# Optimization experiments

Measured on AMD Instinct MI355X. Metric: run time of the kernel, lower is better.

The kernel has to match this reference:

```python
import jax, jax.numpy as jnp
import numpy as np

N = 100000
E = 3200000
IN_DIM = 128
HD = 64
HEADS = 4
NEG_SLOPE = 0.2


def setup_inputs() -> dict:
    key = jax.random.key(0)
    ks = jax.random.split(key, 12)
    s = lambda fan_in: 1.0 / np.sqrt(fan_in)
    x = jax.random.normal(ks[0], (N, IN_DIM), dtype=jnp.float32)
    edge_index = jax.random.randint(ks[1], (2, E), 0, N, dtype=jnp.int64)
    W1 = jax.random.normal(ks[2], (IN_DIM, HEADS * HD), dtype=jnp.float32) * s(IN_DIM)
    a_src1 = jax.random.normal(ks[3], (HEADS, HD), dtype=jnp.float32) * s(HD)
    a_dst1 = jax.random.normal(ks[4], (HEADS, HD), dtype=jnp.float32) * s(HD)
    b1 = jnp.zeros((HEADS * HD,), dtype=jnp.float32)
    W2 = jax.random.normal(ks[5], (HEADS * HD, HD), dtype=jnp.float32) * s(HEADS * HD)
    a_src2 = jax.random.normal(ks[6], (1, HD), dtype=jnp.float32) * s(HD)
    a_dst2 = jax.random.normal(ks[7], (1, HD), dtype=jnp.float32) * s(HD)
    b2 = jnp.zeros((HD,), dtype=jnp.float32)
    lin_w = jax.random.normal(ks[8], (HD, 2), dtype=jnp.float32) * s(HD)
    lin_b = jnp.zeros((2,), dtype=jnp.float32)
    return {"x": x, "edge_index": edge_index, "W1": W1, "a_src1": a_src1,
            "a_dst1": a_dst1, "b1": b1, "W2": W2, "a_src2": a_src2,
            "a_dst2": a_dst2, "b2": b2, "lin_w": lin_w, "lin_b": lin_b}


def gat_conv(x, src, dst, W, a_src, a_dst, bias, heads, out_dim, concat):
    n = x.shape[0]
    h = (x @ W).reshape(n, heads, out_dim)                 # [N,H,D]
    alpha_s = jnp.einsum('nhd,hd->nh', h, a_src)           # [N,H]
    alpha_d = jnp.einsum('nhd,hd->nh', h, a_dst)           # [N,H]
    e = alpha_s[src] + alpha_d[dst]                        # [Etot,H]
    e = jnp.where(e > 0, e, NEG_SLOPE * e)                 # leaky relu
    m = jax.ops.segment_max(e, dst, num_segments=n)        # scatter-softmax (stable)
    m = jnp.where(jnp.isfinite(m), m, 0.0)
    e = jnp.exp(e - m[dst])
    denom = jax.ops.segment_sum(e, dst, num_segments=n)
    alpha = e / denom[dst]                                 # [Etot,H]
    out = jax.ops.segment_sum(h[src] * alpha[:, :, None], dst, num_segments=n)  # [N,H,D]
    out = out.reshape(n, heads * out_dim) if concat else out.mean(axis=1)
    return out + bias


def reference(x, edge_index, W1, a_src1, a_dst1, b1, W2, a_src2, a_dst2, b2, lin_w, lin_b):
    n = x.shape[0]
    loops = jnp.arange(n, dtype=edge_index.dtype)
    src = jnp.concatenate([edge_index[0], loops])          # add self-loops (PyG default)
    dst = jnp.concatenate([edge_index[1], loops])
    h = gat_conv(x, src, dst, W1, a_src1, a_dst1, b1, HEADS, HD, True)
    h = jax.nn.elu(h)
    h = gat_conv(h, src, dst, W2, a_src2, a_dst2, b2, 1, HD, True)
    h = jax.nn.elu(h)
    return h @ lin_w + lin_b                               # [N,2]
```

## Files before the change

kernel.cpp:

```cpp
#include <hip/hip_runtime.h>
#include <hip/hip_fp16.h>
#include <math.h>

#define NN 100000
#define EE 3200000
#define ETOT (EE + NN)
#define NEG_SLOPE 0.2f
#define DMAX 96
#define CHUNK 4096
#define NB0 ((ETOT + CHUNK - 1) / CHUNK)
#define RB 391
#define CAP 16384
#define PREPB 391

typedef _Float16 half8 __attribute__((ext_vector_type(8)));
typedef _Float16 half4v __attribute__((ext_vector_type(4)));
typedef _Float16 half2v __attribute__((ext_vector_type(2)));
typedef float floatx4 __attribute__((ext_vector_type(4)));

__device__ __forceinline__ float wsum64(float v) {
#pragma unroll
  for (int o = 32; o; o >>= 1) v += __shfl_xor(v, o);
  return v;
}
__device__ __forceinline__ float lrelu(float v) { return v > 0.f ? v : NEG_SLOPE * v; }
__device__ __forceinline__ float elu1(float v) { return v > 0.f ? v : expm1f(v); }

__global__ void k_init(int* __restrict__ ccur) {
  ccur[threadIdx.x] = threadIdx.x * CAP;
}

__global__ __launch_bounds__(256) void k_pass1(const int* __restrict__ ei,
                                               int* __restrict__ ccur,
                                               unsigned* __restrict__ ebuf,
                                               const float* __restrict__ W1,
                                               const float* __restrict__ W2,
                                               _Float16* __restrict__ W1t,
                                               _Float16* __restrict__ W2t,
                                               const float* __restrict__ x,
                                               const float* __restrict__ a_src1,
                                               const float* __restrict__ a_dst1,
                                               _Float16* __restrict__ xh,
                                               float* __restrict__ as1,
                                               float* __restrict__ ad1) {
  __shared__ __align__(16) char smem[26624];
  const int b = blockIdx.x;
  const int t = threadIdx.x;
  if (b < NB0) {
    unsigned* vv = (unsigned*)smem;
    unsigned short* cbv = (unsigned short*)(smem + 16384);
    int* h = (int*)(smem + 24576);
    int* cur = (int*)(smem + 25600);
    h[t] = 0;
    __syncthreads();
    int base = b * CHUNK;
    int lim = base + CHUNK; if (lim > ETOT) lim = ETOT;
    int cnt = lim - base;
    for (int i = t; i < cnt; i += 256) {
      int e = base + i;
      int s, d;
      if (e < EE) { s = ei[e]; d = ei[EE + e]; } else { s = e - EE; d = s; }
      unsigned cb = (unsigned)d / (unsigned)RB;
      unsigned dloc = (unsigned)d - cb * (unsigned)RB;
      vv[i] = (dloc << 17) | (unsigned)s;
      cbv[i] = (unsigned short)cb;
      atomicAdd(&h[cb], 1);
    }
    __syncthreads();
    if (h[t]) cur[t] = atomicAdd(&ccur[t], h[t]);
    __syncthreads();
    for (int i = t; i < cnt; i += 256) {
      int cb = cbv[i];
      int pos = atomicAdd(&cur[cb], 1);
      ebuf[pos] = vv[i];
    }
    return;
  }
  if (b < NB0 + 192) {
    int idx = (b - NB0) * 256 + t;
    if (idx < 32768) {
      int n = idx >> 7, k = idx & 127;
      W1t[idx] = (_Float16)W1[k * 256 + n];
    } else {
      int j = idx - 32768;
      int n = j >> 8, k = j & 255;
      W2t[j] = (_Float16)W2[k * 64 + n];
    }
    return;
  }
  float* vs = (float*)smem;
  float* vd = vs + 512;
  for (int i = t; i < 512; i += 256) {
    int h = i >> 7, k = i & 127;
    const float* wrow = W1 + (size_t)k * 256 + h * 64;
    float ss = 0.f, dd = 0.f;
#pragma unroll 8
    for (int d2 = 0; d2 < 64; ++d2) {
      float wv = wrow[d2];
      ss = fmaf(wv, a_src1[h * 64 + d2], ss);
      dd = fmaf(wv, a_dst1[h * 64 + d2], dd);
    }
    vs[i] = ss; vd[i] = dd;
  }
  __syncthreads();
  const int lane = t & 63;
  const int gw = (b - NB0 - 192) * 4 + (t >> 6);
  for (int n = gw; n < NN; n += 4 * PREPB) {
    float2 xv = *(const float2*)(x + (size_t)n * 128 + lane * 2);
    half2v hx; hx[0] = (_Float16)xv.x; hx[1] = (_Float16)xv.y;
    *(half2v*)(xh + (size_t)n * 128 + lane * 2) = hx;
    float p[8];
#pragma unroll
    for (int h = 0; h < 4; ++h) {
      p[h]     = xv.x * vs[h * 128 + lane * 2] + xv.y * vs[h * 128 + lane * 2 + 1];
      p[4 + h] = xv.x * vd[h * 128 + lane * 2] + xv.y * vd[h * 128 + lane * 2 + 1];
    }
#pragma unroll
    for (int j = 0; j < 8; ++j) p[j] = wsum64(p[j]);
    if (lane == 0) {
      *(float4*)(as1 + n * 4) = make_float4(p[0], p[1], p[2], p[3]);
      *(float4*)(ad1 + n * 4) = make_float4(p[4], p[5], p[6], p[7]);
    }
  }
}

__global__ __launch_bounds__(256) void k_pass2(const unsigned* __restrict__ ebuf,
                                               const int* __restrict__ ccur,
                                               int* __restrict__ offs,
                                               int* __restrict__ degarr,
                                               int* __restrict__ csr) {
  __shared__ unsigned ed[CAP];
  __shared__ int hist[RB];
  __shared__ int cur[RB];
  int b = blockIdx.x, t = threadIdx.x;
  int d0 = b * RB;
  int rb = NN - d0; if (rb > RB) rb = RB;
  int w0 = b * CAP;
  int cnt = ccur[b] - w0;
  if (cnt > CAP) cnt = CAP;
  for (int j = t; j < rb; j += 256) hist[j] = 0;
  __syncthreads();
  for (int i = t; i < cnt; i += 256) {
    unsigned v = ebuf[w0 + i];
    ed[i] = v;
    atomicAdd(&hist[v >> 17], 1);
  }
  __syncthreads();
  if (t == 0) {
    int run = w0;
    for (int j = 0; j < rb; ++j) { cur[j] = run; run += hist[j]; }
  }
  __syncthreads();
  for (int j = t; j < rb; j += 256) {
    offs[d0 + j] = cur[j];
    degarr[d0 + j] = hist[j];
  }
  __syncthreads();
  for (int i = t; i < cnt; i += 256) {
    unsigned v = ed[i];
    int pos = atomicAdd(&cur[v >> 17], 1);
    csr[pos] = (int)(v & 0x1FFFFu);
  }
}

__global__ __launch_bounds__(256) void k_agg1(const int* __restrict__ offs,
                                              const int* __restrict__ degarr,
                                              const int* __restrict__ csr_src,
                                              const float* __restrict__ a_s,
                                              const float* __restrict__ a_d,
                                              const _Float16* __restrict__ xh,
                                              _Float16* __restrict__ agg) {
  __shared__ __align__(16) float alp[4][DMAX][4];
  __shared__ int sidx[4][DMAX];
  const int wid = threadIdx.x >> 6;
  const int n = blockIdx.x * 4 + wid;
  const int lane = threadIdx.x & 63;
  const int beg = offs[n], deg = degarr[n];
  const float4 ad = *(const float4*)(a_d + n * 4);
  float4 sm = make_float4(0.f, 0.f, 0.f, 0.f);
  for (int d = lane; d < deg; d += 64) {
    int s = csr_src[beg + d];
    float4 as = *(const float4*)(a_s + s * 4);
    float e0 = __expf(lrelu(as.x + ad.x));
    float e1 = __expf(lrelu(as.y + ad.y));
    float e2 = __expf(lrelu(as.z + ad.z));
    float e3 = __expf(lrelu(as.w + ad.w));
    sm.x += e0; sm.y += e1; sm.z += e2; sm.w += e3;
    if (d < DMAX) {
      sidx[wid][d] = s;
      *(float4*)&alp[wid][d][0] = make_float4(e0, e1, e2, e3);
    }
  }
  sm.x = wsum64(sm.x); sm.y = wsum64(sm.y); sm.z = wsum64(sm.z); sm.w = wsum64(sm.w);
  const float4 inv4 = make_float4(1.f / sm.x, 1.f / sm.y, 1.f / sm.z, 1.f / sm.w);
  const int dlim = deg < DMAX ? deg : DMAX;
  for (int d = lane; d < dlim; d += 64) {
    float4 a = *(float4*)&alp[wid][d][0];
    a.x *= inv4.x; a.y *= inv4.y; a.z *= inv4.z; a.w *= inv4.w;
    *(float4*)&alp[wid][d][0] = a;
  }
  const int g = lane >> 4;
  const int sub = lane & 15;
  const _Float16* __restrict__ hb = xh + sub * 8;
  float acc[4][8];
#pragma unroll
  for (int h = 0; h < 4; ++h)
#pragma unroll
    for (int j = 0; j < 8; ++j) acc[h][j] = 0.f;
  int d = 0;
  for (; d + 8 <= dlim; d += 8) {
    int i0 = d + g, i1 = d + 4 + g;
    int s0 = sidx[wid][i0], s1 = sidx[wid][i1];
    float4 w0 = *(float4*)&alp[wid][i0][0];
    float4 w1 = *(float4*)&alp[wid][i1][0];
    half8 r0 = *(const half8*)(hb + (size_t)s0 * 128);
    half8 r1 = *(const half8*)(hb + (size_t)s1 * 128);
#pragma unroll
    for (int j = 0; j < 8; ++j) {
      float f0 = (float)r0[j], f1 = (float)r1[j];
      acc[0][j] = fmaf(f0, w0.x, acc[0][j]);
      acc[1][j] = fmaf(f0, w0.y, acc[1][j]);
      acc[2][j] = fmaf(f0, w0.z, acc[2][j]);
      acc[3][j] = fmaf(f0, w0.w, acc[3][j]);
      acc[0][j] = fmaf(f1, w1.x, acc[0][j]);
      acc[1][j] = fmaf(f1, w1.y, acc[1][j]);
      acc[2][j] = fmaf(f1, w1.z, acc[2][j]);
      acc[3][j] = fmaf(f1, w1.w, acc[3][j]);
    }
  }
  if (d + 4 <= dlim) {
    int i0 = d + g;
    int s0 = sidx[wid][i0];
    float4 w0 = *(float4*)&alp[wid][i0][0];
    half8 r0 = *(const half8*)(hb + (size_t)s0 * 128);
#pragma unroll
    for (int j = 0; j < 8; ++j) {
      float f0 = (float)r0[j];
      acc[0][j] = fmaf(f0, w0.x, acc[0][j]);
      acc[1][j] = fmaf(f0, w0.y, acc[1][j]);
      acc[2][j] = fmaf(f0, w0.z, acc[2][j]);
      acc[3][j] = fmaf(f0, w0.w, acc[3][j]);
    }
    d += 4;
  }
  if (d < dlim) {
    int idx = d + g;
    bool v = idx < dlim;
    int s = sidx[wid][v ? idx : d];
    float4 w0 = *(float4*)&alp[wid][v ? idx : d][0];
    if (!v) { w0.x = 0.f; w0.y = 0.f; w0.z = 0.f; w0.w = 0.f; }
    half8 r0 = *(const half8*)(hb + (size_t)s * 128);
#pragma unroll
    for (int j = 0; j < 8; ++j) {
      float f0 = (float)r0[j];
      acc[0][j] = fmaf(f0, w0.x, acc[0][j]);
      acc[1][j] = fmaf(f0, w0.y, acc[1][j]);
      acc[2][j] = fmaf(f0, w0.z, acc[2][j]);
      acc[3][j] = fmaf(f0, w0.w, acc[3][j]);
    }
  }
  if (deg > DMAX) {
    for (int dd = DMAX + g; dd < deg; dd += 4) {
      int s = csr_src[beg + dd];
      float4 as = *(const float4*)(a_s + s * 4);
      float w0x = __expf(lrelu(as.x + ad.x)) * inv4.x;
      float w0y = __expf(lrelu(as.y + ad.y)) * inv4.y;
      float w0z = __expf(lrelu(as.z + ad.z)) * inv4.z;
      float w0w = __expf(lrelu(as.w + ad.w)) * inv4.w;
      half8 r0 = *(const half8*)(hb + (size_t)s * 128);
#pragma unroll
      for (int j = 0; j < 8; ++j) {
        float f0 = (float)r0[j];
        acc[0][j] = fmaf(f0, w0x, acc[0][j]);
        acc[1][j] = fmaf(f0, w0y, acc[1][j]);
        acc[2][j] = fmaf(f0, w0z, acc[2][j]);
        acc[3][j] = fmaf(f0, w0w, acc[3][j]);
      }
    }
  }
#pragma unroll
  for (int h = 0; h < 4; ++h)
#pragma unroll
    for (int j = 0; j < 8; ++j) {
      acc[h][j] += __shfl_xor(acc[h][j], 16);
      acc[h][j] += __shfl_xor(acc[h][j], 32);
    }
  if (g == 0) {
#pragma unroll
    for (int h = 0; h < 4; ++h) {
      half8 o;
#pragma unroll
      for (int j = 0; j < 8; ++j) o[j] = (_Float16)acc[h][j];
      *(half8*)(agg + ((size_t)n * 4 + h) * 128 + sub * 8) = o;
    }
  }
}

__global__ __launch_bounds__(256) void k_gemmAgg2(const _Float16* __restrict__ agg,
                                                  const _Float16* __restrict__ W1t,
                                                  const _Float16* __restrict__ W2t,
                                                  const float* __restrict__ b1,
                                                  const float* __restrict__ a_src2,
                                                  const float* __restrict__ a_dst2,
                                                  _Float16* __restrict__ h2h,
                                                  float* __restrict__ as_out,
                                                  float* __restrict__ ad_out) {
  __shared__ _Float16 h1eT[64][264];
  const int tid = threadIdx.x;
  const int row0 = blockIdx.x * 64;
  const int wid = tid >> 6, lane = tid & 63;
  const int m16 = lane & 15, quad = lane >> 4;
  floatx4 acc1[4][4];
#pragma unroll
  for (int h = 0; h < 4; ++h)
#pragma unroll
    for (int nt = 0; nt < 4; ++nt) acc1[h][nt] = (floatx4){0.f, 0.f, 0.f, 0.f};
  const size_t arow = (size_t)(row0 + wid * 16 + m16) * 512;
#pragma unroll
  for (int h = 0; h < 4; ++h) {
#pragma unroll
    for (int ks = 0; ks < 4; ++ks) {
      half8 av = *(const half8*)(agg + arow + h * 128 + ks * 32 + quad * 8);
#pragma unroll
      for (int nt = 0; nt < 4; ++nt) {
        half8 bv = *(const half8*)(W1t + (size_t)(h * 64 + nt * 16 + m16) * 128 + ks * 32 + quad * 8);
        acc1[h][nt] = __builtin_amdgcn_mfma_f32_16x16x32_f16(av, bv, acc1[h][nt], 0, 0, 0);
      }
    }
  }
#pragma unroll
  for (int h = 0; h < 4; ++h)
#pragma unroll
    for (int nt = 0; nt < 4; ++nt) {
      float bb = b1[h * 64 + nt * 16 + m16];
#pragma unroll
      for (int r = 0; r < 4; ++r)
        h1eT[wid * 16 + quad * 4 + r][h * 64 + nt * 16 + m16] = (_Float16)elu1(acc1[h][nt][r] + bb);
    }
  __syncthreads();
  floatx4 acc2[4];
#pragma unroll
  for (int nt = 0; nt < 4; ++nt) acc2[nt] = (floatx4){0.f, 0.f, 0.f, 0.f};
#pragma unroll
  for (int ks = 0; ks < 8; ++ks) {
    half8 av = *(const half8*)&h1eT[wid * 16 + m16][ks * 32 + quad * 8];
#pragma unroll
    for (int nt = 0; nt < 4; ++nt) {
      half8 bv = *(const half8*)(W2t + (size_t)(nt * 16 + m16) * 256 + ks * 32 + quad * 8);
      acc2[nt] = __builtin_amdgcn_mfma_f32_16x16x32_f16(av, bv, acc2[nt], 0, 0, 0);
    }
  }
  float asr[4], adr[4];
#pragma unroll
  for (int nt = 0; nt < 4; ++nt) {
    asr[nt] = a_src2[nt * 16 + m16];
    adr[nt] = a_dst2[nt * 16 + m16];
  }
#pragma unroll
  for (int r = 0; r < 4; ++r) {
    float ps = 0.f, pd = 0.f;
#pragma unroll
    for (int nt = 0; nt < 4; ++nt) {
      ps = fmaf(acc2[nt][r], asr[nt], ps);
      pd = fmaf(acc2[nt][r], adr[nt], pd);
    }
#pragma unroll
    for (int o = 1; o < 16; o <<= 1) { ps += __shfl_xor(ps, o); pd += __shfl_xor(pd, o); }
    int gr = row0 + wid * 16 + quad * 4 + r;
    if (gr < NN) {
      if (m16 == 0) { as_out[gr] = ps; ad_out[gr] = pd; }
#pragma unroll
      for (int nt = 0; nt < 4; ++nt)
        h2h[(size_t)gr * 64 + nt * 16 + m16] = (_Float16)acc2[nt][r];
    }
  }
}

__global__ __launch_bounds__(256) void k_attn2(const int* __restrict__ offs,
                                               const int* __restrict__ degarr,
                                               const int* __restrict__ csr_src,
                                               const float* __restrict__ a_s,
                                               const float* __restrict__ a_d,
                                               const _Float16* __restrict__ h2h,
                                               const float* __restrict__ b2,
                                               const float* __restrict__ lin_w,
                                               const float* __restrict__ lin_b,
                                               float* __restrict__ out) {
  __shared__ float alpha2[4][DMAX];
  __shared__ int sidx2[4][DMAX];
  const int wid = threadIdx.x >> 6;
  const int n = blockIdx.x * 4 + wid;
  const int lane = threadIdx.x & 63;
  const int beg = offs[n], deg = degarr[n];
  const float adn = a_d[n];
  float sm = 0.f;
  for (int d = lane; d < deg; d += 64) {
    int s = csr_src[beg + d];
    float e = __expf(lrelu(a_s[s] + adn));
    sm += e;
    if (d < DMAX) { sidx2[wid][d] = s; alpha2[wid][d] = e; }
  }
  sm = wsum64(sm);
  const float inv = 1.f / sm;
  const int dlim = deg < DMAX ? deg : DMAX;
  for (int d = lane; d < dlim; d += 64) alpha2[wid][d] *= inv;
  const int g = lane >> 4;
  const int sub = lane & 15;
  const _Float16* __restrict__ hb = h2h + sub * 4;
  float a0 = 0.f, a1 = 0.f, a2 = 0.f, a3 = 0.f;
  int d = 0;
  for (; d + 8 <= dlim; d += 8) {
    int i0 = d + g, i1 = d + 4 + g;
    int s0 = sidx2[wid][i0], s1 = sidx2[wid][i1];
    float w0 = alpha2[wid][i0], w1 = alpha2[wid][i1];
    half4v r0 = *(const half4v*)(hb + (size_t)s0 * 64);
    half4v r1 = *(const half4v*)(hb + (size_t)s1 * 64);
    a0 = fmaf((float)r0[0], w0, a0); a1 = fmaf((float)r0[1], w0, a1);
    a2 = fmaf((float)r0[2], w0, a2); a3 = fmaf((float)r0[3], w0, a3);
    a0 = fmaf((float)r1[0], w1, a0); a1 = fmaf((float)r1[1], w1, a1);
    a2 = fmaf((float)r1[2], w1, a2); a3 = fmaf((float)r1[3], w1, a3);
  }
  if (d + 4 <= dlim) {
    int i0 = d + g;
    int s0 = sidx2[wid][i0];
    float w0 = alpha2[wid][i0];
    half4v r0 = *(const half4v*)(hb + (size_t)s0 * 64);
    a0 = fmaf((float)r0[0], w0, a0); a1 = fmaf((float)r0[1], w0, a1);
    a2 = fmaf((float)r0[2], w0, a2); a3 = fmaf((float)r0[3], w0, a3);
    d += 4;
  }
  if (d < dlim) {
    int idx = d + g;
    bool v = idx < dlim;
    int s = sidx2[wid][v ? idx : d];
    float w = v ? alpha2[wid][idx] : 0.f;
    half4v r = *(const half4v*)(hb + (size_t)s * 64);
    a0 = fmaf((float)r[0], w, a0); a1 = fmaf((float)r[1], w, a1);
    a2 = fmaf((float)r[2], w, a2); a3 = fmaf((float)r[3], w, a3);
  }
  if (deg > DMAX && g == 0) {
    for (int dd = DMAX; dd < deg; ++dd) {
      int s = csr_src[beg + dd];
      float w = __expf(lrelu(a_s[s] + adn)) * inv;
      half4v r = *(const half4v*)(hb + (size_t)s * 64);
      a0 = fmaf((float)r[0], w, a0); a1 = fmaf((float)r[1], w, a1);
      a2 = fmaf((float)r[2], w, a2); a3 = fmaf((float)r[3], w, a3);
    }
  }
  a0 += __shfl_xor(a0, 16); a1 += __shfl_xor(a1, 16);
  a2 += __shfl_xor(a2, 16); a3 += __shfl_xor(a3, 16);
  a0 += __shfl_xor(a0, 32); a1 += __shfl_xor(a1, 32);
  a2 += __shfl_xor(a2, 32); a3 += __shfl_xor(a3, 32);
  const int c = sub * 4;
  float4 bb = *(const float4*)(b2 + c);
  float o0 = elu1(a0 + bb.x);
  float o1 = elu1(a1 + bb.y);
  float o2 = elu1(a2 + bb.z);
  float o3 = elu1(a3 + bb.w);
  float4 lw0 = *(const float4*)(lin_w + c * 2);
  float4 lw1 = *(const float4*)(lin_w + c * 2 + 4);
  float p0 = o0 * lw0.x + o1 * lw0.z + o2 * lw1.x + o3 * lw1.z;
  float p1 = o0 * lw0.y + o1 * lw0.w + o2 * lw1.y + o3 * lw1.w;
  p0 = wsum64(p0) * 0.25f;
  p1 = wsum64(p1) * 0.25f;
  if (lane == 0) {
    out[n * 2 + 0] = p0 + lin_b[0];
    out[n * 2 + 1] = p1 + lin_b[1];
  }
}

extern "C" void kernel_launch(void* const* d_in, const int* in_sizes, int n_in,
                              void* d_out, int out_size, void* d_ws, size_t ws_size,
                              hipStream_t stream) {
  const float* x      = (const float*)d_in[0];
  const int*   ei     = (const int*)d_in[1];
  const float* W1     = (const float*)d_in[2];
  const float* a_src1 = (const float*)d_in[3];
  const float* a_dst1 = (const float*)d_in[4];
  const float* b1     = (const float*)d_in[5];
  const float* W2     = (const float*)d_in[6];
  const float* a_src2 = (const float*)d_in[7];
  const float* a_dst2 = (const float*)d_in[8];
  const float* b2     = (const float*)d_in[9];
  const float* lin_w  = (const float*)d_in[10];
  const float* lin_b  = (const float*)d_in[11];
  float* outp = (float*)d_out;

  char* w = (char*)d_ws;
  _Float16* agg  = (_Float16*)(w + 0);
  unsigned* ebuf = (unsigned*)(w + 33554432);
  _Float16* xh   = (_Float16*)(w + 102432768);
  _Float16* h2h  = (_Float16*)(w + 102432768);
  int*    csr    = (int*)(w + 128032768);
  _Float16* W1t  = (_Float16*)(w + 144809984);
  _Float16* W2t  = (_Float16*)(w + 144875520);
  float*  as1    = (float*)(w + 144908288);
  float*  ad1    = (float*)(w + 146508288);
  float*  as2    = (float*)(w + 148108288);
  float*  ad2    = (float*)(w + 148508288);
  int*    offs   = (int*)(w + 148908288);
  int*    degarr = (int*)(w + 149308288);
  int*    ccur   = (int*)(w + 149708288);

  k_init<<<1, 256, 0, stream>>>(ccur);
  k_pass1<<<NB0 + 192 + PREPB, 256, 0, stream>>>(ei, ccur, ebuf, W1, W2, W1t, W2t,
                                                 x, a_src1, a_dst1, xh, as1, ad1);
  k_pass2<<<256, 256, 0, stream>>>(ebuf, ccur, offs, degarr, csr);

  k_agg1<<<NN / 4, 256, 0, stream>>>(offs, degarr, csr, as1, ad1, xh, agg);
  k_gemmAgg2<<<1563, 256, 0, stream>>>(agg, W1t, W2t, b1, a_src2, a_dst2, h2h, as2, ad2);

  k_attn2<<<NN / 4, 256, 0, stream>>>(offs, degarr, csr, as2, ad2, h2h, b2, lin_w, lin_b, outp);
}
```

Before: 594.2 us.

## Fuse layer-1 aggregation with both dense GEMMs into one kernel via LDS

```diff
diff --git a/kernel.cpp b/kernel.cpp
--- a/kernel.cpp
+++ b/kernel.cpp
@@ -163,216 +163,198 @@
   }
 }
 
-__global__ __launch_bounds__(256) void k_agg1(const int* __restrict__ offs,
-                                              const int* __restrict__ degarr,
-                                              const int* __restrict__ csr_src,
-                                              const float* __restrict__ a_s,
-                                              const float* __restrict__ a_d,
-                                              const _Float16* __restrict__ xh,
-                                              _Float16* __restrict__ agg) {
+__global__ __launch_bounds__(256) void k_fused1(const int* __restrict__ offs,
+                                                const int* __restrict__ degarr,
+                                                const int* __restrict__ csr_src,
+                                                const float* __restrict__ a_s,
+                                                const float* __restrict__ a_d,
+                                                const _Float16* __restrict__ xh,
+                                                const _Float16* __restrict__ W1t,
+                                                const _Float16* __restrict__ W2t,
+                                                const float* __restrict__ b1,
+                                                const float* __restrict__ a_src2,
+                                                const float* __restrict__ a_dst2,
+                                                _Float16* __restrict__ h2h,
+                                                float* __restrict__ as_out,
+                                                float* __restrict__ ad_out) {
   __shared__ __align__(16) float alp[4][DMAX][4];
   __shared__ int sidx[4][DMAX];
+  __shared__ __align__(16) _Float16 aggT[16][520];
+  __shared__ __align__(16) _Float16 h1eT[16][264];
+  __shared__ float prt[2][4][16];
   const int wid = threadIdx.x >> 6;
-  const int n = blockIdx.x * 4 + wid;
   const int lane = threadIdx.x & 63;
-  const int beg = offs[n], deg = degarr[n];
-  const float4 ad = *(const float4*)(a_d + n * 4);
-  float4 sm = make_float4(0.f, 0.f, 0.f, 0.f);
-  for (int d = lane; d < deg; d += 64) {
-    int s = csr_src[beg + d];
-    float4 as = *(const float4*)(a_s + s * 4);
-    float e0 = __expf(lrelu(as.x + ad.x));
-    float e1 = __expf(lrelu(as.y + ad.y));
-    float e2 = __expf(lrelu(as.z + ad.z));
-    float e3 = __expf(lrelu(as.w + ad.w));
-    sm.x += e0; sm.y += e1; sm.z += e2; sm.w += e3;
-    if (d < DMAX) {
-      sidx[wid][d] = s;
-      *(float4*)&alp[wid][d][0] = make_float4(e0, e1, e2, e3);
-    }
-  }
-  sm.x = wsum64(sm.x); sm.y = wsum64(sm.y); sm.z = wsum64(sm.z); sm.w = wsum64(sm.w);
-  const float4 inv4 = make_float4(1.f / sm.x, 1.f / sm.y, 1.f / sm.z, 1.f / sm.w);
-  const int dlim = deg < DMAX ? deg : DMAX;
-  for (int d = lane; d < dlim; d += 64) {
-    float4 a = *(float4*)&alp[wid][d][0];
-    a.x *= inv4.x; a.y *= inv4.y; a.z *= inv4.z; a.w *= inv4.w;
-    *(float4*)&alp[wid][d][0] = a;
-  }
+  const int n0 = blockIdx.x * 16;
   const int g = lane >> 4;
   const int sub = lane & 15;
   const _Float16* __restrict__ hb = xh + sub * 8;
-  float acc[4][8];
-#pragma unroll
-  for (int h = 0; h < 4; ++h)
-#pragma unroll
-    for (int j = 0; j < 8; ++j) acc[h][j] = 0.f;
-  int d = 0;
-  for (; d + 8 <= dlim; d += 8) {
-    int i0 = d + g, i1 = d + 4 + g;
-    int s0 = sidx[wid][i0], s1 = sidx[wid][i1];
-    float4 w0 = *(float4*)&alp[wid][i0][0];
-    float4 w1 = *(float4*)&alp[wid][i1][0];
-    half8 r0 = *(const half8*)(hb + (size_t)s0 * 128);
-    half8 r1 = *(const half8*)(hb + (size_t)s1 * 128);
-#pragma unroll
-    for (int j = 0; j < 8; ++j) {
-      float f0 = (float)r0[j], f1 = (float)r1[j];
-      acc[0][j] = fmaf(f0, w0.x, acc[0][j]);
-      acc[1][j] = fmaf(f0, w0.y, acc[1][j]);
-      acc[2][j] = fmaf(f0, w0.z, acc[2][j]);
-      acc[3][j] = fmaf(f0, w0.w, acc[3][j]);
-      acc[0][j] = fmaf(f1, w1.x, acc[0][j]);
-      acc[1][j] = fmaf(f1, w1.y, acc[1][j]);
-      acc[2][j] = fmaf(f1, w1.z, acc[2][j]);
-      acc[3][j] = fmaf(f1, w1.w, acc[3][j]);
-    }
-  }
-  if (d + 4 <= dlim) {
-    int i0 = d + g;
-    int s0 = sidx[wid][i0];
-    float4 w0 = *(float4*)&alp[wid][i0][0];
-    half8 r0 = *(const half8*)(hb + (size_t)s0 * 128);
-#pragma unroll
-    for (int j = 0; j < 8; ++j) {
-      float f0 = (float)r0[j];
-      acc[0][j] = fmaf(f0, w0.x, acc[0][j]);
-      acc[1][j] = fmaf(f0, w0.y, acc[1][j]);
-      acc[2][j] = fmaf(f0, w0.z, acc[2][j]);
-      acc[3][j] = fmaf(f0, w0.w, acc[3][j]);
-    }
-    d += 4;
-  }
-  if (d < dlim) {
-    int idx = d + g;
-    bool v = idx < dlim;
-    int s = sidx[wid][v ? idx : d];
-    float4 w0 = *(float4*)&alp[wid][v ? idx : d][0];
-    if (!v) { w0.x = 0.f; w0.y = 0.f; w0.z = 0.f; w0.w = 0.f; }
-    half8 r0 = *(const half8*)(hb + (size_t)s * 128);
-#pragma unroll
-    for (int j = 0; j < 8; ++j) {
-      float f0 = (float)r0[j];
-      acc[0][j] = fmaf(f0, w0.x, acc[0][j]);
-      acc[1][j] = fmaf(f0, w0.y, acc[1][j]);
-      acc[2][j] = fmaf(f0, w0.z, acc[2][j]);
-      acc[3][j] = fmaf(f0, w0.w, acc[3][j]);
-    }
-  }
-  if (deg > DMAX) {
-    for (int dd = DMAX + g; dd < deg; dd += 4) {
-      int s = csr_src[beg + dd];
+
+  for (int dn = 0; dn < 4; ++dn) {
+    const int n = n0 + wid * 4 + dn;
+    const int beg = offs[n], deg = degarr[n];
+    const float4 ad = *(const float4*)(a_d + n * 4);
+    float4 sm = make_float4(0.f, 0.f, 0.f, 0.f);
+    for (int d = lane; d < deg; d += 64) {
+      int s = csr_src[beg + d];
       float4 as = *(const float4*)(a_s + s * 4);
-      float w0x = __expf(lrelu(as.x + ad.x)) * inv4.x;
-      float w0y = __expf(lrelu(as.y + ad.y)) * inv4.y;
-      float w0z = __expf(lrelu(as.z + ad.z)) * inv4.z;
-      float w0w = __expf(lrelu(as.w + ad.w)) * inv4.w;
-      half8 r0 = *(const half8*)(hb + (size_t)s * 128);
+      float e0 = __expf(lrelu(as.x + ad.x));
+      float e1 = __expf(lrelu(as.y + ad.y));
+      float e2 = __expf(lrelu(as.z + ad.z));
+      float e3 = __expf(lrelu(as.w + ad.w));
+      sm.x += e0; sm.y += e1; sm.z += e2; sm.w += e3;
+      if (d < DMAX) {
+        sidx[wid][d] = s;
+        *(float4*)&alp[wid][d][0] = make_float4(e0, e1, e2, e3);
+      }
+    }
+    sm.x = wsum64(sm.x); sm.y = wsum64(sm.y); sm.z = wsum64(sm.z); sm.w = wsum64(sm.w);
+    const float4 inv4 = make_float4(1.f / sm.x, 1.f / sm.y, 1.f / sm.z, 1.f / sm.w);
+    const int dlim = deg < DMAX ? deg : DMAX;
+    for (int d = lane; d < dlim; d += 64) {
+      float4 a = *(float4*)&alp[wid][d][0];
+      a.x *= inv4.x; a.y *= inv4.y; a.z *= inv4.z; a.w *= inv4.w;
+      *(float4*)&alp[wid][d][0] = a;
+    }
+    float acc[4][8];
+#pragma unroll
+    for (int h = 0; h < 4; ++h)
+#pragma unroll
+      for (int j = 0; j < 8; ++j) acc[h][j] = 0.f;
+    int d = 0;
+    for (; d + 8 <= dlim; d += 8) {
+      int i0 = d + g, i1 = d + 4 + g;
+      int s0 = sidx[wid][i0], s1 = sidx[wid][i1];
+      float4 w0 = *(float4*)&alp[wid][i0][0];
+      float4 w1 = *(float4*)&alp[wid][i1][0];
+      half8 r0 = *(const half8*)(hb + (size_t)s0 * 128);
+      half8 r1 = *(const half8*)(hb + (size_t)s1 * 128);
+#pragma unroll
+      for (int j = 0; j < 8; ++j) {
+        float f0 = (float)r0[j], f1 = (float)r1[j];
+        acc[0][j] = fmaf(f0, w0.x, acc[0][j]);
+        acc[1][j] = fmaf(f0, w0.y, acc[1][j]);
+        acc[2][j] = fmaf(f0, w0.z, acc[2][j]);
+        acc[3][j] = fmaf(f0, w0.w, acc[3][j]);
+        acc[0][j] = fmaf(f1, w1.x, acc[0][j]);
+        acc[1][j] = fmaf(f1, w1.y, acc[1][j]);
+        acc[2][j] = fmaf(f1, w1.z, acc[2][j]);
+        acc[3][j] = fmaf(f1, w1.w, acc[3][j]);
+      }
+    }
+    if (d + 4 <= dlim) {
+      int i0 = d + g;
+      int s0 = sidx[wid][i0];
+      float4 w0 = *(float4*)&alp[wid][i0][0];
+      half8 r0 = *(const half8*)(hb + (size_t)s0 * 128);
 #pragma unroll
       for (int j = 0; j < 8; ++j) {
         float f0 = (float)r0[j];
-        acc[0][j] = fmaf(f0, w0x, acc[0][j]);
-        acc[1][j] = fmaf(f0, w0y, acc[1][j]);
-        acc[2][j] = fmaf(f0, w0z, acc[2][j]);
-        acc[3][j] = fmaf(f0, w0w, acc[3][j]);
-      }
-    }
-  }
-#pragma unroll
-  for (int h = 0; h < 4; ++h)
-#pragma unroll
-    for (int j = 0; j < 8; ++j) {
-      acc[h][j] += __shfl_xor(acc[h][j], 16);
-      acc[h][j] += __shfl_xor(acc[h][j], 32);
-    }
-  if (g == 0) {
-#pragma unroll
-    for (int h = 0; h < 4; ++h) {
-      half8 o;
-#pragma unroll
-      for (int j = 0; j < 8; ++j) o[j] = (_Float16)acc[h][j];
-      *(half8*)(agg + ((size_t)n * 4 + h) * 128 + sub * 8) = o;
-    }
-  }
-}
-
-__global__ __launch_bounds__(256) void k_gemmAgg2(const _Float16* __restrict__ agg,
-                                                  const _Float16* __restrict__ W1t,
-                                                  const _Float16* __restrict__ W2t,
-                                                  const float* __restrict__ b1,
-                                                  const float* __restrict__ a_src2,
-                                                  const float* __restrict__ a_dst2,
-                                                  _Float16* __restrict__ h2h,
-                                                  float* __restrict__ as_out,
-                                                  float* __restrict__ ad_out) {
-  __shared__ _Float16 h1eT[64][264];
-  const int tid = threadIdx.x;
-  const int row0 = blockIdx.x * 64;
-  const int wid = tid >> 6, lane = tid & 63;
-  const int m16 = lane & 15, quad = lane >> 4;
-  floatx4 acc1[4][4];
-#pragma unroll
-  for (int h = 0; h < 4; ++h)
-#pragma unroll
-    for (int nt = 0; nt < 4; ++nt) acc1[h][nt] = (floatx4){0.f, 0.f, 0.f, 0.f};
-  const size_t arow = (size_t)(row0 + wid * 16 + m16) * 512;
-#pragma unroll
-  for (int h = 0; h < 4; ++h) {
-#pragma unroll
-    for (int ks = 0; ks < 4; ++ks) {
-      half8 av = *(const half8*)(agg + arow + h * 128 + ks * 32 + quad * 8);
-#pragma unroll
-      for (int nt = 0; nt < 4; ++nt) {
-        half8 bv = *(const half8*)(W1t + (size_t)(h * 64 + nt * 16 + m16) * 128 + ks * 32 + quad * 8);
-        acc1[h][nt] = __builtin_amdgcn_mfma_f32_16x16x32_f16(av, bv, acc1[h][nt], 0, 0, 0);
-      }
-    }
-  }
-#pragma unroll
-  for (int h = 0; h < 4; ++h)
+        acc[0][j] = fmaf(f0, w0.x, acc[0][j]);
+        acc[1][j] = fmaf(f0, w0.y, acc[1][j]);
+        acc[2][j] = fmaf(f0, w0.z, acc[2][j]);
+        acc[3][j] = fmaf(f0, w0.w, acc[3][j]);
+      }
+      d += 4;
+    }
+    if (d < dlim) {
+      int idx = d + g;
+      bool v = idx < dlim;
+      int s = sidx[wid][v ? idx : d];
+      float4 w0 = *(float4*)&alp[wid][v ? idx : d][0];
+      if (!v) { w0.x = 0.f; w0.y = 0.f; w0.z = 0.f; w0.w = 0.f; }
+      half8 r0 = *(const half8*)(hb + (size_t)s * 128);
+#pragma unroll
+      for (int j = 0; j < 8; ++j) {
+        float f0 = (float)r0[j];
+        acc[0][j] = fmaf(f0, w0.x, acc[0][j]);
+        acc[1][j] = fmaf(f0, w0.y, acc[1][j]);
+        acc[2][j] = fmaf(f0, w0.z, acc[2][j]);
+        acc[3][j] = fmaf(f0, w0.w, acc[3][j]);
+      }
+    }
+    if (deg > DMAX) {
+      for (int dd = DMAX + g; dd < deg; dd += 4) {
+        int s = csr_src[beg + dd];
+        float4 as = *(const float4*)(a_s + s * 4);
+        float w0x = __expf(lrelu(as.x + ad.x)) * inv4.x;
+        float w0y = __expf(lrelu(as.y + ad.y)) * inv4.y;
+        float w0z = __expf(lrelu(as.z + ad.z)) * inv4.z;
+        float w0w = __expf(lrelu(as.w + ad.w)) * inv4.w;
+        half8 r0 = *(const half8*)(hb + (size_t)s * 128);
+#pragma unroll
+        for (int j = 0; j < 8; ++j) {
+          float f0 = (float)r0[j];
+          acc[0][j] = fmaf(f0, w0x, acc[0][j]);
+          acc[1][j] = fmaf(f0, w0y, acc[1][j]);
+          acc[2][j] = fmaf(f0, w0z, acc[2][j]);
+          acc[3][j] = fmaf(f0, w0w, acc[3][j]);
+        }
+      }
+    }
+#pragma unroll
+    for (int h = 0; h < 4; ++h)
+#pragma unroll
+      for (int j = 0; j < 8; ++j) {
+        acc[h][j] += __shfl_xor(acc[h][j], 16);
+        acc[h][j] += __shfl_xor(acc[h][j], 32);
+      }
+    if (g == 0) {
+#pragma unroll
+      for (int h = 0; h < 4; ++h) {
+        half8 o;
+#pragma unroll
+        for (int j = 0; j < 8; ++j) o[j] = (_Float16)acc[h][j];
+        *(half8*)&aggT[wid * 4 + dn][h * 128 + sub * 8] = o;
+      }
+    }
+  }
+  __syncthreads();
+
+  const int m16 = sub, quad = g;
+  floatx4 acc1[4];
+#pragma unroll
+  for (int nt = 0; nt < 4; ++nt) acc1[nt] = (floatx4){0.f, 0.f, 0.f, 0.f};
+#pragma unroll
+  for (int ks = 0; ks < 4; ++ks) {
+    half8 av = *(half8*)&aggT[m16][wid * 128 + ks * 32 + quad * 8];
 #pragma unroll
     for (int nt = 0; nt < 4; ++nt) {
-      float bb = b1[h * 64 + nt * 16 + m16];
-#pragma unroll
-      for (int r = 0; r < 4; ++r)
-        h1eT[wid * 16 + quad * 4 + r][h * 64 + nt * 16 + m16] = (_Float16)elu1(acc1[h][nt][r] + bb);
-    }
-  __syncthreads();
-  floatx4 acc2[4];
-#pragma unroll
-  for (int nt = 0; nt < 4; ++nt) acc2[nt] = (floatx4){0.f, 0.f, 0.f, 0.f};
+      half8 bv = *(const half8*)(W1t + (size_t)(wid * 64 + nt * 16 + m16) * 128 + ks * 32 + quad * 8);
+      acc1[nt] = __builtin_amdgcn_mfma_f32_16x16x32_f16(av, bv, acc1[nt], 0, 0, 0);
+    }
+  }
+#pragma unroll
+  for (int nt = 0; nt < 4; ++nt) {
+    float bb = b1[wid * 64 + nt * 16 + m16];
+#pragma unroll
+    for (int r = 0; r < 4; ++r)
+      h1eT[quad * 4 + r][wid * 64 + nt * 16 + m16] = (_Float16)elu1(acc1[nt][r] + bb);
+  }
+  __syncthreads();
+
+  floatx4 acc2 = (floatx4){0.f, 0.f, 0.f, 0.f};
 #pragma unroll
   for (int ks = 0; ks < 8; ++ks) {
-    half8 av = *(const half8*)&h1eT[wid * 16 + m16][ks * 32 + quad * 8];
-#pragma unroll
-    for (int nt = 0; nt < 4; ++nt) {
-      half8 bv = *(const half8*)(W2t + (size_t)(nt * 16 + m16) * 256 + ks * 32 + quad * 8);
-      acc2[nt] = __builtin_amdgcn_mfma_f32_16x16x32_f16(av, bv, acc2[nt], 0, 0, 0);
-    }
-  }
-  float asr[4], adr[4];
-#pragma unroll
-  for (int nt = 0; nt < 4; ++nt) {
-    asr[nt] = a_src2[nt * 16 + m16];
-    adr[nt] = a_dst2[nt * 16 + m16];
-  }
+    half8 av = *(half8*)&h1eT[m16][ks * 32 + quad * 8];
+    half8 bv = *(const half8*)(W2t + (size_t)(wid * 16 + m16) * 256 + ks * 32 + quad * 8);
+    acc2 = __builtin_amdgcn_mfma_f32_16x16x32_f16(av, bv, acc2, 0, 0, 0);
+  }
+  const float a2v = a_src2[wid * 16 + m16];
+  const float d2v = a_dst2[wid * 16 + m16];
 #pragma unroll
   for (int r = 0; r < 4; ++r) {
-    float ps = 0.f, pd = 0.f;
-#pragma unroll
-    for (int nt = 0; nt < 4; ++nt) {
-      ps = fmaf(acc2[nt][r], asr[nt], ps);
-      pd = fmaf(acc2[nt][r], adr[nt], pd);
-    }
+    int row = quad * 4 + r;
+    h2h[(size_t)(n0 + row) * 64 + wid * 16 + m16] = (_Float16)acc2[r];
+    float ps = acc2[r] * a2v, pd = acc2[r] * d2v;
 #pragma unroll
     for (int o = 1; o < 16; o <<= 1) { ps += __shfl_xor(ps, o); pd += __shfl_xor(pd, o); }
-    int gr = row0 + wid * 16 + quad * 4 + r;
-    if (gr < NN) {
-      if (m16 == 0) { as_out[gr] = ps; ad_out[gr] = pd; }
-#pragma unroll
-      for (int nt = 0; nt < 4; ++nt)
-        h2h[(size_t)gr * 64 + nt * 16 + m16] = (_Float16)acc2[nt][r];
-    }
+    if (m16 == 0) { prt[0][wid][row] = ps; prt[1][wid][row] = pd; }
+  }
+  __syncthreads();
+  if (threadIdx.x < 16) {
+    int row = threadIdx.x;
+    as_out[n0 + row] = prt[0][0][row] + prt[0][1][row] + prt[0][2][row] + prt[0][3][row];
+    ad_out[n0 + row] = prt[1][0][row] + prt[1][1][row] + prt[1][2][row] + prt[1][3][row];
   }
 }
 
@@ -487,28 +469,27 @@
   float* outp = (float*)d_out;
 
   char* w = (char*)d_ws;
-  _Float16* agg  = (_Float16*)(w + 0);
-  unsigned* ebuf = (unsigned*)(w + 33554432);
-  _Float16* xh   = (_Float16*)(w + 102432768);
-  _Float16* h2h  = (_Float16*)(w + 102432768);
-  int*    csr    = (int*)(w + 128032768);
-  _Float16* W1t  = (_Float16*)(w + 144809984);
-  _Float16* W2t  = (_Float16*)(w + 144875520);
-  float*  as1    = (float*)(w + 144908288);
-  float*  ad1    = (float*)(w + 146508288);
-  float*  as2    = (float*)(w + 148108288);
-  float*  ad2    = (float*)(w + 148508288);
-  int*    offs   = (int*)(w + 148908288);
-  int*    degarr = (int*)(w + 149308288);
-  int*    ccur   = (int*)(w + 149708288);
+  _Float16* xh   = (_Float16*)(w + 0);
+  _Float16* h2h  = (_Float16*)(w + 25600000);
+  unsigned* ebuf = (unsigned*)(w + 38400000);
+  int*    csr    = (int*)(w + 55177216);
+  _Float16* W1t  = (_Float16*)(w + 71954432);
+  _Float16* W2t  = (_Float16*)(w + 72019968);
+  float*  as1    = (float*)(w + 72052736);
+  float*  ad1    = (float*)(w + 73652736);
+  float*  as2    = (float*)(w + 75252736);
+  float*  ad2    = (float*)(w + 75652736);
+  int*    offs   = (int*)(w + 76052736);
+  int*    degarr = (int*)(w + 76452736);
+  int*    ccur   = (int*)(w + 76852736);
 
   k_init<<<1, 256, 0, stream>>>(ccur);
   k_pass1<<<NB0 + 192 + PREPB, 256, 0, stream>>>(ei, ccur, ebuf, W1, W2, W1t, W2t,
                                                  x, a_src1, a_dst1, xh, as1, ad1);
   k_pass2<<<256, 256, 0, stream>>>(ebuf, ccur, offs, degarr, csr);
 
-  k_agg1<<<NN / 4, 256, 0, stream>>>(offs, degarr, csr, as1, ad1, xh, agg);
-  k_gemmAgg2<<<1563, 256, 0, stream>>>(agg, W1t, W2t, b1, a_src2, a_dst2, h2h, as2, ad2);
+  k_fused1<<<NN / 16, 256, 0, stream>>>(offs, degarr, csr, as1, ad1, xh,
+                                        W1t, W2t, b1, a_src2, a_dst2, h2h, as2, ad2);
 
   k_attn2<<<NN / 4, 256, 0, stream>>>(offs, degarr, csr, as2, ad2, h2h, b2, lin_w, lin_b, outp);
 }
```

Result: faster. 551.7 us (-7.2%).

## Restructure gemmAgg2 into 32-row tiles staged in LDS and vectorize x prep

Applied to the files above, without the earlier changes.

```diff
diff --git a/kernel.cpp b/kernel.cpp
--- a/kernel.cpp
+++ b/kernel.cpp
@@ -15,7 +15,6 @@
 
 typedef _Float16 half8 __attribute__((ext_vector_type(8)));
 typedef _Float16 half4v __attribute__((ext_vector_type(4)));
-typedef _Float16 half2v __attribute__((ext_vector_type(2)));
 typedef float floatx4 __attribute__((ext_vector_type(4)));
 
 __device__ __forceinline__ float wsum64(float v) {
@@ -104,20 +103,44 @@
   }
   __syncthreads();
   const int lane = t & 63;
+  const int sub8 = lane >> 3;
+  const int dl = lane & 7;
   const int gw = (b - NB0 - 192) * 4 + (t >> 6);
-  for (int n = gw; n < NN; n += 4 * PREPB) {
-    float2 xv = *(const float2*)(x + (size_t)n * 128 + lane * 2);
-    half2v hx; hx[0] = (_Float16)xv.x; hx[1] = (_Float16)xv.y;
-    *(half2v*)(xh + (size_t)n * 128 + lane * 2) = hx;
+  for (int nb = gw * 8; nb < NN; nb += 4 * PREPB * 8) {
+    const int n = nb + sub8;
+    const bool ok = n < NN;
+    float4 xv[4];
+#pragma unroll
+    for (int j = 0; j < 4; ++j)
+      xv[j] = ok ? *(const float4*)(x + (size_t)n * 128 + dl * 16 + j * 4)
+                 : make_float4(0.f, 0.f, 0.f, 0.f);
+    const float* xf = (const float*)xv;
+    if (ok) {
+      half8 h0, h1;
+#pragma unroll
+      for (int c = 0; c < 8; ++c) { h0[c] = (_Float16)xf[c]; h1[c] = (_Float16)xf[8 + c]; }
+      *(half8*)(xh + (size_t)n * 128 + dl * 16) = h0;
+      *(half8*)(xh + (size_t)n * 128 + dl * 16 + 8) = h1;
+    }
     float p[8];
 #pragma unroll
     for (int h = 0; h < 4; ++h) {
-      p[h]     = xv.x * vs[h * 128 + lane * 2] + xv.y * vs[h * 128 + lane * 2 + 1];
-      p[4 + h] = xv.x * vd[h * 128 + lane * 2] + xv.y * vd[h * 128 + lane * 2 + 1];
-    }
-#pragma unroll
-    for (int j = 0; j < 8; ++j) p[j] = wsum64(p[j]);
-    if (lane == 0) {
+      float ss = 0.f, dd = 0.f;
+#pragma unroll
+      for (int c = 0; c < 16; ++c) {
+        float xc = xf[c];
+        ss = fmaf(xc, vs[h * 128 + dl * 16 + c], ss);
+        dd = fmaf(xc, vd[h * 128 + dl * 16 + c], dd);
+      }
+      p[h] = ss; p[4 + h] = dd;
+    }
+#pragma unroll
+    for (int j = 0; j < 8; ++j) {
+      p[j] += __shfl_xor(p[j], 1);
+      p[j] += __shfl_xor(p[j], 2);
+      p[j] += __shfl_xor(p[j], 4);
+    }
+    if (ok && dl == 0) {
       *(float4*)(as1 + n * 4) = make_float4(p[0], p[1], p[2], p[3]);
       *(float4*)(ad1 + n * 4) = make_float4(p[4], p[5], p[6], p[7]);
     }
@@ -305,74 +328,77 @@
                                                   _Float16* __restrict__ h2h,
                                                   float* __restrict__ as_out,
                                                   float* __restrict__ ad_out) {
-  __shared__ _Float16 h1eT[64][264];
+  __shared__ __align__(16) _Float16 As[32][520];
+  __shared__ __align__(16) _Float16 h1eT[32][264];
+  __shared__ float prt[2][4][32];
   const int tid = threadIdx.x;
-  const int row0 = blockIdx.x * 64;
+  const int row0 = blockIdx.x * 32;
+#pragma unroll
+  for (int i = 0; i < 8; ++i) {
+    int c = i * 256 + tid;
+    int r = c >> 6;
+    int c8 = c & 63;
+    *(half8*)&As[r][c8 * 8] = *(const half8*)(agg + (size_t)(row0 + r) * 512 + c8 * 8);
+  }
+  __syncthreads();
   const int wid = tid >> 6, lane = tid & 63;
   const int m16 = lane & 15, quad = lane >> 4;
-  floatx4 acc1[4][4];
-#pragma unroll
-  for (int h = 0; h < 4; ++h)
-#pragma unroll
-    for (int nt = 0; nt < 4; ++nt) acc1[h][nt] = (floatx4){0.f, 0.f, 0.f, 0.f};
-  const size_t arow = (size_t)(row0 + wid * 16 + m16) * 512;
-#pragma unroll
-  for (int h = 0; h < 4; ++h) {
+  floatx4 acc1[2][4];
+#pragma unroll
+  for (int mt = 0; mt < 2; ++mt)
+#pragma unroll
+    for (int nt = 0; nt < 4; ++nt) acc1[mt][nt] = (floatx4){0.f, 0.f, 0.f, 0.f};
+#pragma unroll
+  for (int mt = 0; mt < 2; ++mt) {
 #pragma unroll
     for (int ks = 0; ks < 4; ++ks) {
-      half8 av = *(const half8*)(agg + arow + h * 128 + ks * 32 + quad * 8);
+      half8 av = *(half8*)&As[mt * 16 + m16][wid * 128 + ks * 32 + quad * 8];
 #pragma unroll
       for (int nt = 0; nt < 4; ++nt) {
-        half8 bv = *(const half8*)(W1t + (size_t)(h * 64 + nt * 16 + m16) * 128 + ks * 32 + quad * 8);
-        acc1[h][nt] = __builtin_amdgcn_mfma_f32_16x16x32_f16(av, bv, acc1[h][nt], 0, 0, 0);
+        half8 bv = *(const half8*)(W1t + (size_t)(wid * 64 + nt * 16 + m16) * 128 + ks * 32 + quad * 8);
+        acc1[mt][nt] = __builtin_amdgcn_mfma_f32_16x16x32_f16(av, bv, acc1[mt][nt], 0, 0, 0);
       }
     }
   }
 #pragma unroll
-  for (int h = 0; h < 4; ++h)
+  for (int mt = 0; mt < 2; ++mt)
 #pragma unroll
     for (int nt = 0; nt < 4; ++nt) {
-      float bb = b1[h * 64 + nt * 16 + m16];
+      float bb = b1[wid * 64 + nt * 16 + m16];
 #pragma unroll
       for (int r = 0; r < 4; ++r)
-        h1eT[wid * 16 + quad * 4 + r][h * 64 + nt * 16 + m16] = (_Float16)elu1(acc1[h][nt][r] + bb);
-    }
-  __syncthreads();
-  floatx4 acc2[4];
-#pragma unroll
-  for (int nt = 0; nt < 4; ++nt) acc2[nt] = (floatx4){0.f, 0.f, 0.f, 0.f};
-#pragma unroll
-  for (int ks = 0; ks < 8; ++ks) {
-    half8 av = *(const half8*)&h1eT[wid * 16 + m16][ks * 32 + quad * 8];
-#pragma unroll
-    for (int nt = 0; nt < 4; ++nt) {
-      half8 bv = *(const half8*)(W2t + (size_t)(nt * 16 + m16) * 256 + ks * 32 + quad * 8);
-      acc2[nt] = __builtin_amdgcn_mfma_f32_16x16x32_f16(av, bv, acc2[nt], 0, 0, 0);
-    }
-  }
-  float asr[4], adr[4];
-#pragma unroll
-  for (int nt = 0; nt < 4; ++nt) {
-    asr[nt] = a_src2[nt * 16 + m16];
-    adr[nt] = a_dst2[nt * 16 + m16];
-  }
-#pragma unroll
-  for (int r = 0; r < 4; ++r) {
-    float ps = 0.f, pd = 0.f;
-#pragma unroll
-    for (int nt = 0; nt < 4; ++nt) {
-      ps = fmaf(acc2[nt][r], asr[nt], ps);
-      pd = fmaf(acc2[nt][r], adr[nt], pd);
-    }
-#pragma unroll
-    for (int o = 1; o < 16; o <<= 1) { ps += __shfl_xor(ps, o); pd += __shfl_xor(pd, o); }
-    int gr = row0 + wid * 16 + quad * 4 + r;
-    if (gr < NN) {
-      if (m16 == 0) { as_out[gr] = ps; ad_out[gr] = pd; }
-#pragma unroll
-      for (int nt = 0; nt < 4; ++nt)
-        h2h[(size_t)gr * 64 + nt * 16 + m16] = (_Float16)acc2[nt][r];
-    }
+        h1eT[mt * 16 + quad * 4 + r][wid * 64 + nt * 16 + m16] = (_Float16)elu1(acc1[mt][nt][r] + bb);
+    }
+  __syncthreads();
+  floatx4 acc2[2];
+#pragma unroll
+  for (int mt = 0; mt < 2; ++mt) acc2[mt] = (floatx4){0.f, 0.f, 0.f, 0.f};
+#pragma unroll
+  for (int mt = 0; mt < 2; ++mt) {
+#pragma unroll
+    for (int ks = 0; ks < 8; ++ks) {
+      half8 av = *(half8*)&h1eT[mt * 16 + m16][ks * 32 + quad * 8];
+      half8 bv = *(const half8*)(W2t + (size_t)(wid * 16 + m16) * 256 + ks * 32 + quad * 8);
+      acc2[mt] = __builtin_amdgcn_mfma_f32_16x16x32_f16(av, bv, acc2[mt], 0, 0, 0);
+    }
+  }
+  const float a2v = a_src2[wid * 16 + m16];
+  const float d2v = a_dst2[wid * 16 + m16];
+#pragma unroll
+  for (int mt = 0; mt < 2; ++mt)
+#pragma unroll
+    for (int r = 0; r < 4; ++r) {
+      int row = mt * 16 + quad * 4 + r;
+      h2h[(size_t)(row0 + row) * 64 + wid * 16 + m16] = (_Float16)acc2[mt][r];
+      float ps = acc2[mt][r] * a2v, pd = acc2[mt][r] * d2v;
+#pragma unroll
+      for (int o = 1; o < 16; o <<= 1) { ps += __shfl_xor(ps, o); pd += __shfl_xor(pd, o); }
+      if (m16 == 0) { prt[0][wid][row] = ps; prt[1][wid][row] = pd; }
+    }
+  __syncthreads();
+  if (tid < 32) {
+    as_out[row0 + tid] = prt[0][0][tid] + prt[0][1][tid] + prt[0][2][tid] + prt[0][3][tid];
+    ad_out[row0 + tid] = prt[1][0][tid] + prt[1][1][tid] + prt[1][2][tid] + prt[1][3][tid];
   }
 }
 
@@ -489,18 +515,18 @@
   char* w = (char*)d_ws;
   _Float16* agg  = (_Float16*)(w + 0);
   unsigned* ebuf = (unsigned*)(w + 33554432);
-  _Float16* xh   = (_Float16*)(w + 102432768);
-  _Float16* h2h  = (_Float16*)(w + 102432768);
-  int*    csr    = (int*)(w + 128032768);
-  _Float16* W1t  = (_Float16*)(w + 144809984);
-  _Float16* W2t  = (_Float16*)(w + 144875520);
-  float*  as1    = (float*)(w + 144908288);
-  float*  ad1    = (float*)(w + 146508288);
-  float*  as2    = (float*)(w + 148108288);
-  float*  ad2    = (float*)(w + 148508288);
-  int*    offs   = (int*)(w + 148908288);
-  int*    degarr = (int*)(w + 149308288);
-  int*    ccur   = (int*)(w + 149708288);
+  _Float16* xh   = (_Float16*)(w + 102400000);
+  _Float16* h2h  = (_Float16*)(w + 102400000);
+  int*    csr    = (int*)(w + 128000000);
+  _Float16* W1t  = (_Float16*)(w + 144777216);
+  _Float16* W2t  = (_Float16*)(w + 144842752);
+  float*  as1    = (float*)(w + 144875520);
+  float*  ad1    = (float*)(w + 146475520);
+  float*  as2    = (float*)(w + 148075520);
+  float*  ad2    = (float*)(w + 148475520);
+  int*    offs   = (int*)(w + 148875520);
+  int*    degarr = (int*)(w + 149275520);
+  int*    ccur   = (int*)(w + 149675520);
 
   k_init<<<1, 256, 0, stream>>>(ccur);
   k_pass1<<<NB0 + 192 + PREPB, 256, 0, stream>>>(ei, ccur, ebuf, W1, W2, W1t, W2t,
@@ -508,7 +534,7 @@
   k_pass2<<<256, 256, 0, stream>>>(ebuf, ccur, offs, degarr, csr);
 
   k_agg1<<<NN / 4, 256, 0, stream>>>(offs, degarr, csr, as1, ad1, xh, agg);
-  k_gemmAgg2<<<1563, 256, 0, stream>>>(agg, W1t, W2t, b1, a_src2, a_dst2, h2h, as2, ad2);
+  k_gemmAgg2<<<NN / 32, 256, 0, stream>>>(agg, W1t, W2t, b1, a_src2, a_dst2, h2h, as2, ad2);
 
   k_attn2<<<NN / 4, 256, 0, stream>>>(offs, degarr, csr, as2, ad2, h2h, b2, lin_w, lin_b, outp);
 }
```

Result: faster. 507.7 us (-14.6%).
